# Performance work log

Hardware: AMD Instinct MI355X
Metric: run time of the kernel (lower is better)

## Reference

```python
import jax, jax.numpy as jnp
import numpy as np

DIM = 192
HEADS = 6
WH, WW = 7, 7
N = WH * WW            # 49 tokens per window
NW = 64                # windows per image
B = 64                 # images
B_ = NW * B            # 4096 window-batches
HEAD_DIM = DIM // HEADS
TABLE = (2 * WH - 1) * (2 * WW - 1)  # 169


def _relative_position_index():
    ch, cw = np.meshgrid(np.arange(WH), np.arange(WW), indexing='ij')
    coords = np.stack([ch, cw]).reshape(2, -1)          # (2, N)
    rel = coords[:, :, None] - coords[:, None, :]       # (2, N, N)
    rel = rel.transpose(1, 2, 0).astype(np.int32)
    rel[:, :, 0] += WH - 1
    rel[:, :, 1] += WW - 1
    rel[:, :, 0] *= 2 * WW - 1
    return jnp.asarray(rel.sum(-1))                     # (N, N) int32


def setup_inputs() -> dict:
    key = jax.random.key(0)
    ks = jax.random.split(key, 7)
    x = jax.random.normal(ks[0], (B_, N, DIM), dtype=jnp.float32)
    # 0 / -100 additive window mask (as produced by shifted-window masking)
    m = jax.random.uniform(ks[1], (NW, N, N))
    mask = jnp.where(m < 0.8, 0.0, -100.0).astype(jnp.float32)
    qkv_w = jax.random.normal(ks[2], (3 * DIM, DIM), dtype=jnp.float32) * 0.02
    qkv_b = jnp.zeros((3 * DIM,), dtype=jnp.float32)
    proj_w = jax.random.normal(ks[3], (DIM, DIM), dtype=jnp.float32) * 0.02
    proj_b = jnp.zeros((DIM,), dtype=jnp.float32)
    rpb_table = jax.random.normal(ks[4], (TABLE, HEADS), dtype=jnp.float32) * 0.02
    rel_idx = _relative_position_index()
    return {"x": x, "mask": mask, "qkv_w": qkv_w, "qkv_b": qkv_b,
            "proj_w": proj_w, "proj_b": proj_b, "rpb_table": rpb_table,
            "rel_idx": rel_idx}


def reference(x, mask, qkv_w, qkv_b, proj_w, proj_b, rpb_table, rel_idx):
    Bw, n, c = x.shape
    scale = HEAD_DIM ** -0.5
    qkv = x @ qkv_w.T + qkv_b                                  # (B_, N, 3C)
    qkv = qkv.reshape(Bw, n, 3, HEADS, HEAD_DIM).transpose(2, 0, 3, 1, 4)
    q, k, v = qkv[0], qkv[1], qkv[2]                           # (B_, H, N, hd)
    attn = jnp.einsum('bhid,bhjd->bhij', q * scale, k)          # (B_, H, N, N)
    bias = rpb_table[rel_idx.reshape(-1)].reshape(n, n, HEADS)  # gather
    attn = attn + bias.transpose(2, 0, 1)[None]                 # (1, H, N, N)
    nW = mask.shape[0]
    attn = attn.reshape(Bw // nW, nW, HEADS, n, n) + mask[None, :, None]
    attn = attn.reshape(Bw, HEADS, n, n)
    attn = jax.nn.softmax(attn, axis=-1).astype(v.dtype)
    out = jnp.einsum('bhij,bhjd->bhid', attn, v)                # (B_, H, N, hd)
    out = out.transpose(0, 2, 1, 3).reshape(Bw, n, c)
    return out @ proj_w.T + proj_b
```

## Files before the change

kernel.cpp:

```cpp
#include <hip/hip_runtime.h>

typedef unsigned short u16;
typedef unsigned int   u32;
typedef _Float16 f16x8 __attribute__((ext_vector_type(8)));
typedef __fp16   hf2   __attribute__((ext_vector_type(2)));
typedef float    f32x4 __attribute__((ext_vector_type(4)));

#define NTOK 49
#define CDIM 192
#define NH   6
#define HD   32
#define SC   0.17677669529663687f

#define QOFF   0
#define QSTR   200
#define KOFF   9800
#define VTOFF  19600
#define VTSTR  56
#define POFF   30352
#define PSTR   72
#define ARENA_U16 40152

#define WS_WQ 0
#define WS_WP 110592
#define WS_BM 147456

static __device__ __forceinline__ u16 f2h(float f){ union{ _Float16 h; u16 u;} v; v.h=(_Float16)f; return v.u; }
static __device__ __forceinline__ u32 pk2(float a, float b){
    hf2 h = __builtin_amdgcn_cvt_pkrtz(a, b);
    return __builtin_bit_cast(u32, h);
}

__global__ void prep_weights(const float* __restrict__ qkv_w,
                             const float* __restrict__ proj_w,
                             u16* __restrict__ ws)
{
    const int idx = blockIdx.x*256 + threadIdx.x;
    if (idx < 110592) {
        const int fid = idx >> 9, r = idx & 511;
        const int lane = r >> 3, e = r & 7;
        const int t = fid/6, k6 = fid - 6*t;
        const int col = t*16 + (lane & 15);
        const int kk  = k6*32 + (lane >> 4)*8 + e;
        float w = qkv_w[col*CDIM + kk];
        if (col < CDIM) w *= SC;
        ws[WS_WQ + idx] = f2h(w);
    } else if (idx < 147456) {
        const int j = idx - 110592;
        const int fid = j >> 9, r = j & 511;
        const int lane = r >> 3, e = r & 7;
        const int t = fid/6, k6 = fid - 6*t;
        const int col = t*16 + (lane & 15);
        const int kk  = k6*32 + (lane >> 4)*8 + e;
        ws[WS_WP + j] = f2h(proj_w[col*CDIM + kk]);
    }
}

__global__ void prep_bm(const float* __restrict__ mask,
                        const float* __restrict__ rpb,
                        const int*   __restrict__ rel,
                        u16* __restrict__ ws)
{
    const int idx = blockIdx.x*256 + threadIdx.x;
    if (idx >= 64*NH*256*16) return;
    const int r   = idx & 3;
    const int jt  = (idx >> 2) & 3;
    const int tid = (idx >> 4) & 255;
    const int rest = idx >> 12;
    const int h = rest % NH;
    const int w = rest / NH;
    const int i  = 16*(tid >> 6) + (tid & 15);
    const int lg = (tid >> 4) & 3;
    const int j  = jt*16 + 4*lg + r;
    float v;
    if (i >= NTOK)      v = 0.0f;
    else if (j >= NTOK) v = -1e30f;
    else v = rpb[rel[i*NTOK+j]*NH + h] + mask[((size_t)w*NTOK+i)*NTOK + j];
    ws[WS_BM + idx] = f2h(v);
}

#define LDFRAG(B, BASE, t) { const u16* _p = (BASE) + (size_t)(t)*3072 + lane*8;      \
    B[0]=*(const f16x8*)(_p);      B[1]=*(const f16x8*)(_p+512);                      \
    B[2]=*(const f16x8*)(_p+1024); B[3]=*(const f16x8*)(_p+1536);                     \
    B[4]=*(const f16x8*)(_p+2048); B[5]=*(const f16x8*)(_p+2560); }

#define QKV_STEP(s, CUR, NXT, PF) {                                                   \
    if (PF) LDFRAG(NXT, wq, t0+(s)+1);                                                \
    const int _t = t0+(s); const int _sec = _t/12; const int _cb = (_t - _sec*12)*16; \
    f32x4 _ac[2];                                                                     \
    if (_sec < 2) {       \
      float4 _b4 = *(const float4*)&qkv_b[_t*16 + 4*lg];                              \
      if (_sec == 0) { _b4.x*=SC; _b4.y*=SC; _b4.z*=SC; _b4.w*=SC; }                  \
      const f32x4 _ini = {_b4.x, _b4.y, _b4.z, _b4.w};                                \
      _ac[0]=_ini; _ac[1]=_ini;                                                       \
      _Pragma("unroll") for (int _k=0;_k<6;++_k)                                      \
        _Pragma("unroll") for (int _mi=0;_mi<2;++_mi)                                 \
          _ac[_mi] = __builtin_amdgcn_mfma_f32_16x16x32_f16(CUR[_k], A[_k][_mi], _ac[_mi],0,0,0); \
      u16* _dst = (_sec==0) ? (arena+QOFF) : (arena+KOFF);                            \
      _Pragma("unroll") for (int _mi=0;_mi<2;++_mi) {                                 \
        const int _tok = 32*mg + 16*_mi + l15;                                        \
        if (_tok < NTOK) {                                                            \
          uint2 _wd = make_uint2(pk2(_ac[_mi][0], _ac[_mi][1]),                       \
                                 pk2(_ac[_mi][2], _ac[_mi][3]));                      \
          *(uint2*)&_dst[_tok*QSTR + _cb + 4*lg] = _wd; } }                           \
    } else {                            \
      const float _b1 = qkv_b[384 + _cb + l15];                                       \
      const f32x4 _ini = {_b1, _b1, _b1, _b1};                                        \
      _ac[0]=_ini; _ac[1]=_ini;                                                       \
      _Pragma("unroll") for (int _k=0;_k<6;++_k)                                      \
        _Pragma("unroll") for (int _mi=0;_mi<2;++_mi)                                 \
          _ac[_mi] = __builtin_amdgcn_mfma_f32_16x16x32_f16(A[_k][_mi], CUR[_k], _ac[_mi],0,0,0); \
      _Pragma("unroll") for (int _mi=0;_mi<2;++_mi) {                                 \
        const int _tb = 32*mg + 16*_mi + 4*lg;                                        \
        if (_tb <= 48) {                                                              \
          uint2 _wd = make_uint2(pk2(_ac[_mi][0], _ac[_mi][1]),                       \
                                 pk2(_ac[_mi][2], _ac[_mi][3]));                      \
          *(uint2*)&arena[VTOFF + (_cb + l15)*VTSTR + _tb] = _wd; } } } }

#define PROJ_STEP(s, CUR, NXT, PF) {                                                  \
    if (PF) LDFRAG(NXT, wp, p0+(s)+1);                                                \
    const f32x4 _ini = {pb4[s].x, pb4[s].y, pb4[s].z, pb4[s].w};                      \
    f32x4 _ac[2]; _ac[0]=_ini; _ac[1]=_ini;                                           \
    _Pragma("unroll") for (int _k=0;_k<6;++_k)                                        \
      _Pragma("unroll") for (int _mi=0;_mi<2;++_mi)                                   \
        _ac[_mi] = __builtin_amdgcn_mfma_f32_16x16x32_f16(CUR[_k], PA[_k][_mi], _ac[_mi],0,0,0); \
    _Pragma("unroll") for (int _mi=0;_mi<2;++_mi) {                                   \
      const int _tok = 32*mg + 16*_mi + l15;                                          \
      if (_tok < NTOK) {                                                              \
        float4 _o = make_float4(_ac[_mi][0], _ac[_mi][1], _ac[_mi][2], _ac[_mi][3]);  \
        *(float4*)&og[(size_t)_tok*CDIM + (p0+(s))*16 + 4*lg] = _o; } } }

__global__ __launch_bounds__(512, 4)
void winattn_core(const float* __restrict__ x,
                  const float* __restrict__ qkv_b,
                  const float* __restrict__ proj_b,
                  const u16* __restrict__ ws,
                  float* __restrict__ out)
{
    __shared__ __align__(16) u16 arena[ARENA_U16];
    const int b    = blockIdx.x;
    const int tid  = threadIdx.x;
    const int lane = tid & 63;
    const int wv   = tid >> 6;
    const int rg   = wv & 3;
    const int mg   = wv >> 2;
    const int l15  = lane & 15;
    const int lg   = lane >> 4;
    const int win  = b & 63;

    {
        const float4* xg = (const float4*)(x + (size_t)b * (NTOK * CDIM));
        for (int i = tid; i < NTOK * CDIM / 4; i += 512) {
            const float4 v = xg[i];
            const int row = (i * 4) / CDIM, col = (i * 4) % CDIM;
            *(uint2*)&arena[POFF + row * QSTR + col] =
                make_uint2(pk2(v.x, v.y), pk2(v.z, v.w));
        }
        for (int i = tid; i < CDIM * 4; i += 512)
            arena[VTOFF + (i >> 2) * VTSTR + 52 + (i & 3)] = 0;
    }
    __syncthreads();

    const u16* wq = ws + WS_WQ;
    const int t0 = rg * 9;
    {
        f16x8 A[6][2];
        #pragma unroll
        for (int mi = 0; mi < 2; ++mi) {
            const int r = 32*mg + 16*mi + l15;
            const int ar = (r < NTOK ? r : NTOK-1) * QSTR;
            #pragma unroll
            for (int k6 = 0; k6 < 6; ++k6)
                A[k6][mi] = *(const f16x8*)&arena[POFF + ar + k6*32 + 8*lg];
        }
        f16x8 Ba[6], Bb[6];
        LDFRAG(Ba, wq, t0);
        QKV_STEP(0, Ba, Bb, 1)
        QKV_STEP(1, Bb, Ba, 1)
        QKV_STEP(2, Ba, Bb, 1)
        QKV_STEP(3, Bb, Ba, 1)
        QKV_STEP(4, Ba, Bb, 1)
        QKV_STEP(5, Bb, Ba, 1)
        QKV_STEP(6, Ba, Bb, 1)
        QKV_STEP(7, Bb, Ba, 1)
        QKV_STEP(8, Ba, Bb, 0)
    }

    f16x8 bmf[3][2];
    {
        const u16* bmb = ws + WS_BM + ((((size_t)win*NH + 3*mg)*256) + rg*64 + lane)*16;
        #pragma unroll
        for (int h3 = 0; h3 < 3; ++h3) {
            bmf[h3][0] = *(const f16x8*)(bmb + h3*4096);
            bmf[h3][1] = *(const f16x8*)(bmb + h3*4096 + 8);
        }
    }
    __syncthreads();

    const int i0 = 16 * rg;
    const bool myok = (i0 + l15 < NTOK);
    const int myrow = myok ? i0 + l15 : NTOK-1;
    int krow[4];
    #pragma unroll
    for (int jt = 0; jt < 4; ++jt)
        krow[jt] = (jt*16 + l15 < NTOK ? jt*16 + l15 : NTOK-1) * QSTR;

    f16x8 Qf[3];
    #pragma unroll
    for (int h3 = 0; h3 < 3; ++h3)
        Qf[h3] = *(const f16x8*)&arena[QOFF + myrow*QSTR + (3*mg+h3)*HD + 8*lg];

    u16* pp = arena + POFF + wv*1152;
    const int a1 = (32 + 8*lg <= 48) ? 32 + 8*lg : 48;

    #pragma unroll
    for (int h3 = 0; h3 < 3; ++h3) {
        const int h = 3*mg + h3;
        f32x4 pacc[4];
        #pragma unroll
        for (int jt = 0; jt < 4; ++jt) {
            const f16x8 Kf = *(const f16x8*)&arena[KOFF + krow[jt] + h*HD + 8*lg];
            f32x4 z = {};
            pacc[jt] = __builtin_amdgcn_mfma_f32_16x16x32_f16(Kf, Qf[h3], z, 0, 0, 0);
        }
        float val[4][4]; float mx = -3e38f;
        #pragma unroll
        for (int jt = 0; jt < 4; ++jt)
            #pragma unroll
            for (int r = 0; r < 4; ++r) {
                val[jt][r] = pacc[jt][r] + (float)bmf[h3][jt>>1][(jt&1)*4 + r];
                mx = fmaxf(mx, val[jt][r]);
            }
        mx = fmaxf(mx, __shfl_xor(mx, 16));
        mx = fmaxf(mx, __shfl_xor(mx, 32));
        float s = 0.f;
        #pragma unroll
        for (int jt = 0; jt < 4; ++jt)
            #pragma unroll
            for (int r = 0; r < 4; ++r) { const float e = __expf(val[jt][r]-mx); val[jt][r]=e; s+=e; }
        s += __shfl_xor(s, 16); s += __shfl_xor(s, 32);
        const float inv = 1.0f / s;
        #pragma unroll
        for (int jt = 0; jt < 4; ++jt)
            *(uint2*)&pp[l15*PSTR + jt*16 + 4*lg] =
                make_uint2(pk2(val[jt][0], val[jt][1]), pk2(val[jt][2], val[jt][3]));
        const f16x8 Pb0 = *(const f16x8*)&pp[l15*PSTR + 8*lg];
        const f16x8 Pb1 = *(const f16x8*)&pp[l15*PSTR + 32 + 8*lg];
        #pragma unroll
        for (int nt = 0; nt < 2; ++nt) {
            const int vr = (h*HD + nt*16 + l15) * VTSTR;
            const f16x8 Va0 = *(const f16x8*)&arena[VTOFF + vr + 8*lg];
            const f16x8 Va1 = *(const f16x8*)&arena[VTOFF + vr + a1];
            f32x4 o = {};
            o = __builtin_amdgcn_mfma_f32_16x16x32_f16(Va0, Pb0, o, 0, 0, 0);
            o = __builtin_amdgcn_mfma_f32_16x16x32_f16(Va1, Pb1, o, 0, 0, 0);
            if (myok) {
                *(uint2*)&arena[QOFF + (i0+l15)*QSTR + h*HD + nt*16 + 4*lg] =
                    make_uint2(pk2(o[0]*inv, o[1]*inv), pk2(o[2]*inv, o[3]*inv));
            }
        }
    }

    const u16* wp = ws + WS_WP;
    const int p0 = rg * 3;
    f16x8 Pa[6], Pb2[6];
    LDFRAG(Pa, wp, p0);
    float4 pb4[3];
    #pragma unroll
    for (int s = 0; s < 3; ++s)
        pb4[s] = *(const float4*)&proj_b[(p0+s)*16 + 4*lg];
    __syncthreads();
    {
        f16x8 PA[6][2];
        #pragma unroll
        for (int mi = 0; mi < 2; ++mi) {
            const int r = 32*mg + 16*mi + l15;
            const int ar = (r < NTOK ? r : NTOK-1) * QSTR;
            #pragma unroll
            for (int k6 = 0; k6 < 6; ++k6)
                PA[k6][mi] = *(const f16x8*)&arena[QOFF + ar + k6*32 + 8*lg];
        }
        float* og = out + (size_t)b * (NTOK * CDIM);
        PROJ_STEP(0, Pa, Pb2, 1)
        PROJ_STEP(1, Pb2, Pa, 1)
        PROJ_STEP(2, Pa, Pb2, 0)
    }
}

extern "C" void kernel_launch(void* const* d_in, const int* in_sizes, int n_in,
                              void* d_out, int out_size, void* d_ws, size_t ws_size,
                              hipStream_t stream) {
    const float* x      = (const float*)d_in[0];
    const float* mask   = (const float*)d_in[1];
    const float* qkv_w  = (const float*)d_in[2];
    const float* qkv_b  = (const float*)d_in[3];
    const float* proj_w = (const float*)d_in[4];
    const float* proj_b = (const float*)d_in[5];
    const float* rpb    = (const float*)d_in[6];
    const int*   rel    = (const int*)d_in[7];
    u16* ws = (u16*)d_ws;

    const int nwin = in_sizes[0] / (NTOK * CDIM);
    prep_weights<<<576, 256, 0, stream>>>(qkv_w, proj_w, ws);
    prep_bm<<<(64*NH*256*16 + 255)/256, 256, 0, stream>>>(mask, rpb, rel, ws);
    winattn_core<<<nwin, 512, 0, stream>>>(x, qkv_b, proj_b, ws, (float*)d_out);
}
```

Before: 185.1 us.

## Load x fragments directly from global, drop staging barrier, add MFMA priority hints

Input rows are now converted from global fp32 straight into MFMA A-fragments in registers. This removes the shared-memory staging of x and the __syncthreads that followed it, and it shrinks the LDS arena, which may allow higher occupancy. Bias is added after the MFMA chain instead of being used as the accumulator init, and sched_barrier plus s_setprio calls wrap the MFMA blocks so matrix work is prioritised over other waves. The trade-off is that each wave re-reads overlapping x rows from global memory, with less coalesced access and extra conversion work.

```diff
diff --git a/kernel.cpp b/kernel.cpp
--- a/kernel.cpp
+++ b/kernel.cpp
@@ -19,7 +19,7 @@
 #define VTSTR  56
 #define POFF   30352
 #define PSTR   72
-#define ARENA_U16 40152
+#define ARENA_U16 39568
 
 #define WS_WQ 0
 #define WS_WP 110592
@@ -85,45 +85,51 @@
     B[4]=*(const f16x8*)(_p+2048); B[5]=*(const f16x8*)(_p+2560); }
 
 #define QKV_STEP(s, CUR, NXT, PF) {                                                   \
-    if (PF) LDFRAG(NXT, wq, t0+(s)+1);                                                \
     const int _t = t0+(s); const int _sec = _t/12; const int _cb = (_t - _sec*12)*16; \
-    f32x4 _ac[2];                                                                     \
-    if (_sec < 2) {       \
-      float4 _b4 = *(const float4*)&qkv_b[_t*16 + 4*lg];                              \
-      if (_sec == 0) { _b4.x*=SC; _b4.y*=SC; _b4.z*=SC; _b4.w*=SC; }                  \
-      const f32x4 _ini = {_b4.x, _b4.y, _b4.z, _b4.w};                                \
-      _ac[0]=_ini; _ac[1]=_ini;                                                       \
+    if (PF) { LDFRAG(NXT, wq, t0+(s)+1); }                                            \
+    float4 _b4; float _b1;                                                            \
+    if (_sec < 2) { _b4 = *(const float4*)&qkv_b[_t*16 + 4*lg];                       \
+                    if (_sec == 0) { _b4.x*=SC; _b4.y*=SC; _b4.z*=SC; _b4.w*=SC; } }  \
+    else          { _b1 = qkv_b[384 + _cb + l15]; }                                   \
+    __builtin_amdgcn_sched_barrier(0);                                                \
+    f32x4 _ac[2] = {};                                                                \
+    __builtin_amdgcn_s_setprio(1);                                                    \
+    if (_sec < 2) {                         \
       _Pragma("unroll") for (int _k=0;_k<6;++_k)                                      \
         _Pragma("unroll") for (int _mi=0;_mi<2;++_mi)                                 \
           _ac[_mi] = __builtin_amdgcn_mfma_f32_16x16x32_f16(CUR[_k], A[_k][_mi], _ac[_mi],0,0,0); \
+    } else {                            \
+      _Pragma("unroll") for (int _k=0;_k<6;++_k)                                      \
+        _Pragma("unroll") for (int _mi=0;_mi<2;++_mi)                                 \
+          _ac[_mi] = __builtin_amdgcn_mfma_f32_16x16x32_f16(A[_k][_mi], CUR[_k], _ac[_mi],0,0,0); \
+    }                                                                                 \
+    __builtin_amdgcn_s_setprio(0);                                                    \
+    if (_sec < 2) {                                                                   \
       u16* _dst = (_sec==0) ? (arena+QOFF) : (arena+KOFF);                            \
       _Pragma("unroll") for (int _mi=0;_mi<2;++_mi) {                                 \
         const int _tok = 32*mg + 16*_mi + l15;                                        \
         if (_tok < NTOK) {                                                            \
-          uint2 _wd = make_uint2(pk2(_ac[_mi][0], _ac[_mi][1]),                       \
-                                 pk2(_ac[_mi][2], _ac[_mi][3]));                      \
+          uint2 _wd = make_uint2(pk2(_ac[_mi][0]+_b4.x, _ac[_mi][1]+_b4.y),           \
+                                 pk2(_ac[_mi][2]+_b4.z, _ac[_mi][3]+_b4.w));          \
           *(uint2*)&_dst[_tok*QSTR + _cb + 4*lg] = _wd; } }                           \
-    } else {                            \
-      const float _b1 = qkv_b[384 + _cb + l15];                                       \
-      const f32x4 _ini = {_b1, _b1, _b1, _b1};                                        \
-      _ac[0]=_ini; _ac[1]=_ini;                                                       \
-      _Pragma("unroll") for (int _k=0;_k<6;++_k)                                      \
-        _Pragma("unroll") for (int _mi=0;_mi<2;++_mi)                                 \
-          _ac[_mi] = __builtin_amdgcn_mfma_f32_16x16x32_f16(A[_k][_mi], CUR[_k], _ac[_mi],0,0,0); \
+    } else {                                                                          \
       _Pragma("unroll") for (int _mi=0;_mi<2;++_mi) {                                 \
         const int _tb = 32*mg + 16*_mi + 4*lg;                                        \
         if (_tb <= 48) {                                                              \
-          uint2 _wd = make_uint2(pk2(_ac[_mi][0], _ac[_mi][1]),                       \
-                                 pk2(_ac[_mi][2], _ac[_mi][3]));                      \
+          uint2 _wd = make_uint2(pk2(_ac[_mi][0]+_b1, _ac[_mi][1]+_b1),               \
+                                 pk2(_ac[_mi][2]+_b1, _ac[_mi][3]+_b1));              \
           *(uint2*)&arena[VTOFF + (_cb + l15)*VTSTR + _tb] = _wd; } } } }
 
 #define PROJ_STEP(s, CUR, NXT, PF) {                                                  \
-    if (PF) LDFRAG(NXT, wp, p0+(s)+1);                                                \
+    if (PF) { LDFRAG(NXT, wp, p0+(s)+1); }                                            \
+    __builtin_amdgcn_sched_barrier(0);                                                \
     const f32x4 _ini = {pb4[s].x, pb4[s].y, pb4[s].z, pb4[s].w};                      \
     f32x4 _ac[2]; _ac[0]=_ini; _ac[1]=_ini;                                           \
+    __builtin_amdgcn_s_setprio(1);                                                    \
     _Pragma("unroll") for (int _k=0;_k<6;++_k)                                        \
       _Pragma("unroll") for (int _mi=0;_mi<2;++_mi)                                   \
         _ac[_mi] = __builtin_amdgcn_mfma_f32_16x16x32_f16(CUR[_k], PA[_k][_mi], _ac[_mi],0,0,0); \
+    __builtin_amdgcn_s_setprio(0);                                                    \
     _Pragma("unroll") for (int _mi=0;_mi<2;++_mi) {                                   \
       const int _tok = 32*mg + 16*_mi + l15;                                          \
       if (_tok < NTOK) {                                                              \
@@ -148,33 +154,31 @@
     const int lg   = lane >> 4;
     const int win  = b & 63;
 
-    {
-        const float4* xg = (const float4*)(x + (size_t)b * (NTOK * CDIM));
-        for (int i = tid; i < NTOK * CDIM / 4; i += 512) {
-            const float4 v = xg[i];
-            const int row = (i * 4) / CDIM, col = (i * 4) % CDIM;
-            *(uint2*)&arena[POFF + row * QSTR + col] =
-                make_uint2(pk2(v.x, v.y), pk2(v.z, v.w));
-        }
-        for (int i = tid; i < CDIM * 4; i += 512)
-            arena[VTOFF + (i >> 2) * VTSTR + 52 + (i & 3)] = 0;
-    }
-    __syncthreads();
+    for (int i = tid; i < CDIM * 4; i += 512)
+        arena[VTOFF + (i >> 2) * VTSTR + 52 + (i & 3)] = 0;
 
     const u16* wq = ws + WS_WQ;
     const int t0 = rg * 9;
     {
-        f16x8 A[6][2];
-        #pragma unroll
-        for (int mi = 0; mi < 2; ++mi) {
-            const int r = 32*mg + 16*mi + l15;
-            const int ar = (r < NTOK ? r : NTOK-1) * QSTR;
-            #pragma unroll
-            for (int k6 = 0; k6 < 6; ++k6)
-                A[k6][mi] = *(const f16x8*)&arena[POFF + ar + k6*32 + 8*lg];
-        }
         f16x8 Ba[6], Bb[6];
         LDFRAG(Ba, wq, t0);
+        f16x8 A[6][2];
+        {
+            const float* xb = x + (size_t)b * (NTOK * CDIM);
+            #pragma unroll
+            for (int mi = 0; mi < 2; ++mi) {
+                const int r = 32*mg + 16*mi + l15;
+                const float* xr = xb + (size_t)(r < NTOK ? r : NTOK-1) * CDIM;
+                #pragma unroll
+                for (int k6 = 0; k6 < 6; ++k6) {
+                    const float4 f0 = *(const float4*)&xr[k6*32 + 8*lg];
+                    const float4 f1 = *(const float4*)&xr[k6*32 + 8*lg + 4];
+                    const uint4 u = make_uint4(pk2(f0.x,f0.y), pk2(f0.z,f0.w),
+                                               pk2(f1.x,f1.y), pk2(f1.z,f1.w));
+                    A[k6][mi] = __builtin_bit_cast(f16x8, u);
+                }
+            }
+        }
         QKV_STEP(0, Ba, Bb, 1)
         QKV_STEP(1, Bb, Ba, 1)
         QKV_STEP(2, Ba, Bb, 1)
@@ -246,17 +250,23 @@
                 make_uint2(pk2(val[jt][0], val[jt][1]), pk2(val[jt][2], val[jt][3]));
         const f16x8 Pb0 = *(const f16x8*)&pp[l15*PSTR + 8*lg];
         const f16x8 Pb1 = *(const f16x8*)&pp[l15*PSTR + 32 + 8*lg];
+        __builtin_amdgcn_s_setprio(1);
+        f32x4 o[2];
         #pragma unroll
         for (int nt = 0; nt < 2; ++nt) {
             const int vr = (h*HD + nt*16 + l15) * VTSTR;
             const f16x8 Va0 = *(const f16x8*)&arena[VTOFF + vr + 8*lg];
             const f16x8 Va1 = *(const f16x8*)&arena[VTOFF + vr + a1];
-            f32x4 o = {};
-            o = __builtin_amdgcn_mfma_f32_16x16x32_f16(Va0, Pb0, o, 0, 0, 0);
-            o = __builtin_amdgcn_mfma_f32_16x16x32_f16(Va1, Pb1, o, 0, 0, 0);
+            f32x4 z = {};
+            z = __builtin_amdgcn_mfma_f32_16x16x32_f16(Va0, Pb0, z, 0, 0, 0);
+            o[nt] = __builtin_amdgcn_mfma_f32_16x16x32_f16(Va1, Pb1, z, 0, 0, 0);
+        }
+        __builtin_amdgcn_s_setprio(0);
+        #pragma unroll
+        for (int nt = 0; nt < 2; ++nt) {
             if (myok) {
                 *(uint2*)&arena[QOFF + (i0+l15)*QSTR + h*HD + nt*16 + 4*lg] =
-                    make_uint2(pk2(o[0]*inv, o[1]*inv), pk2(o[2]*inv, o[3]*inv));
+                    make_uint2(pk2(o[nt][0]*inv, o[nt][1]*inv), pk2(o[nt][2]*inv, o[nt][3]*inv));
             }
         }
     }
@@ -269,17 +279,20 @@
     #pragma unroll
     for (int s = 0; s < 3; ++s)
         pb4[s] = *(const float4*)&proj_b[(p0+s)*16 + 4*lg];
+    int arow[2];
+    #pragma unroll
+    for (int mi = 0; mi < 2; ++mi) {
+        const int r = 32*mg + 16*mi + l15;
+        arow[mi] = (r < NTOK ? r : NTOK-1) * QSTR;
+    }
     __syncthreads();
     {
         f16x8 PA[6][2];
         #pragma unroll
-        for (int mi = 0; mi < 2; ++mi) {
-            const int r = 32*mg + 16*mi + l15;
-            const int ar = (r < NTOK ? r : NTOK-1) * QSTR;
+        for (int mi = 0; mi < 2; ++mi)
             #pragma unroll
             for (int k6 = 0; k6 < 6; ++k6)
-                PA[k6][mi] = *(const f16x8*)&arena[QOFF + ar + k6*32 + 8*lg];
-        }
+                PA[k6][mi] = *(const f16x8*)&arena[QOFF + arow[mi] + k6*32 + 8*lg];
         float* og = out + (size_t)b * (NTOK * CDIM);
         PROJ_STEP(0, Pa, Pb2, 1)
         PROJ_STEP(1, Pb2, Pa, 1)
```

After: 319.0 us. 72.3% more time.

## Halve block to 256 threads, deepen weight prefetch to three stages

Applied to the files above, without the earlier changes.

The fused window-attention kernel drops from 8 to 4 waves per block. Each wave now handles 18 QKV column tiles and 6 projection tiles, and in the attention phase it processes all 6 heads for one 16-row query tile. Weight fragments are prefetched three tiles ahead using four rotating register buffers instead of double buffering, so global-load latency is better hidden. The change also increases register pressure and lowers launch bounds to 256 threads with 2 blocks per SIMD, which cuts per-block parallelism and may reduce occupancy.

```diff
diff --git a/kernel.cpp b/kernel.cpp
--- a/kernel.cpp
+++ b/kernel.cpp
@@ -17,7 +17,7 @@
 #define KOFF   9800
 #define VTOFF  19600
 #define VTSTR  56
-#define POFF   30352
+#define XOFF   30352
 #define PSTR   72
 #define ARENA_U16 40152
 
@@ -85,7 +85,7 @@
     B[4]=*(const f16x8*)(_p+2048); B[5]=*(const f16x8*)(_p+2560); }
 
 #define QKV_STEP(s, CUR, NXT, PF) {                                                   \
-    if (PF) LDFRAG(NXT, wq, t0+(s)+1);                                                \
+    if (PF) { LDFRAG(NXT, wq, t0+(s)+3); }                                            \
     const int _t = t0+(s); const int _sec = _t/12; const int _cb = (_t - _sec*12)*16; \
     f32x4 _ac[2];                                                                     \
     if (_sec < 2) {       \
@@ -118,8 +118,9 @@
           *(uint2*)&arena[VTOFF + (_cb + l15)*VTSTR + _tb] = _wd; } } } }
 
 #define PROJ_STEP(s, CUR, NXT, PF) {                                                  \
-    if (PF) LDFRAG(NXT, wp, p0+(s)+1);                                                \
-    const f32x4 _ini = {pb4[s].x, pb4[s].y, pb4[s].z, pb4[s].w};                      \
+    if (PF) { LDFRAG(NXT, wp, p0+(s)+3); }                                            \
+    const float4 _pb = *(const float4*)&proj_b[(p0+(s))*16 + 4*lg];                   \
+    const f32x4 _ini = {_pb.x, _pb.y, _pb.z, _pb.w};                                  \
     f32x4 _ac[2]; _ac[0]=_ini; _ac[1]=_ini;                                           \
     _Pragma("unroll") for (int _k=0;_k<6;++_k)                                        \
       _Pragma("unroll") for (int _mi=0;_mi<2;++_mi)                                   \
@@ -130,7 +131,7 @@
         float4 _o = make_float4(_ac[_mi][0], _ac[_mi][1], _ac[_mi][2], _ac[_mi][3]);  \
         *(float4*)&og[(size_t)_tok*CDIM + (p0+(s))*16 + 4*lg] = _o; } } }
 
-__global__ __launch_bounds__(512, 4)
+__global__ __launch_bounds__(256, 2)
 void winattn_core(const float* __restrict__ x,
                   const float* __restrict__ qkv_b,
                   const float* __restrict__ proj_b,
@@ -142,27 +143,31 @@
     const int tid  = threadIdx.x;
     const int lane = tid & 63;
     const int wv   = tid >> 6;
-    const int rg   = wv & 3;
-    const int mg   = wv >> 2;
+    const int mg   = wv >> 1;
+    const int ng   = wv & 1;
     const int l15  = lane & 15;
     const int lg   = lane >> 4;
     const int win  = b & 63;
 
+    const u16* wq = ws + WS_WQ;
+    const int t0 = ng * 18;
+
+    f16x8 B0[6], B1[6], B2[6], B3[6];
+    LDFRAG(B0, wq, t0); LDFRAG(B1, wq, t0+1); LDFRAG(B2, wq, t0+2);
+
     {
         const float4* xg = (const float4*)(x + (size_t)b * (NTOK * CDIM));
-        for (int i = tid; i < NTOK * CDIM / 4; i += 512) {
+        for (int i = tid; i < NTOK * CDIM / 4; i += 256) {
             const float4 v = xg[i];
             const int row = (i * 4) / CDIM, col = (i * 4) % CDIM;
-            *(uint2*)&arena[POFF + row * QSTR + col] =
+            *(uint2*)&arena[XOFF + row * QSTR + col] =
                 make_uint2(pk2(v.x, v.y), pk2(v.z, v.w));
         }
-        for (int i = tid; i < CDIM * 4; i += 512)
-            arena[VTOFF + (i >> 2) * VTSTR + 52 + (i & 3)] = 0;
+        for (int i = tid; i < CDIM * 7; i += 256)
+            arena[VTOFF + (i / 7) * VTSTR + 49 + (i % 7)] = 0;
     }
     __syncthreads();
 
-    const u16* wq = ws + WS_WQ;
-    const int t0 = rg * 9;
     {
         f16x8 A[6][2];
         #pragma unroll
@@ -171,33 +176,40 @@
             const int ar = (r < NTOK ? r : NTOK-1) * QSTR;
             #pragma unroll
             for (int k6 = 0; k6 < 6; ++k6)
-                A[k6][mi] = *(const f16x8*)&arena[POFF + ar + k6*32 + 8*lg];
-        }
-        f16x8 Ba[6], Bb[6];
-        LDFRAG(Ba, wq, t0);
-        QKV_STEP(0, Ba, Bb, 1)
-        QKV_STEP(1, Bb, Ba, 1)
-        QKV_STEP(2, Ba, Bb, 1)
-        QKV_STEP(3, Bb, Ba, 1)
-        QKV_STEP(4, Ba, Bb, 1)
-        QKV_STEP(5, Bb, Ba, 1)
-        QKV_STEP(6, Ba, Bb, 1)
-        QKV_STEP(7, Bb, Ba, 1)
-        QKV_STEP(8, Ba, Bb, 0)
-    }
-
-    f16x8 bmf[3][2];
+                A[k6][mi] = *(const f16x8*)&arena[XOFF + ar + k6*32 + 8*lg];
+        }
+        QKV_STEP( 0, B0, B3, 1)
+        QKV_STEP( 1, B1, B0, 1)
+        QKV_STEP( 2, B2, B1, 1)
+        QKV_STEP( 3, B3, B2, 1)
+        QKV_STEP( 4, B0, B3, 1)
+        QKV_STEP( 5, B1, B0, 1)
+        QKV_STEP( 6, B2, B1, 1)
+        QKV_STEP( 7, B3, B2, 1)
+        QKV_STEP( 8, B0, B3, 1)
+        QKV_STEP( 9, B1, B0, 1)
+        QKV_STEP(10, B2, B1, 1)
+        QKV_STEP(11, B3, B2, 1)
+        QKV_STEP(12, B0, B3, 1)
+        QKV_STEP(13, B1, B0, 1)
+        QKV_STEP(14, B2, B1, 1)
+        QKV_STEP(15, B3, B2, 0)
+        QKV_STEP(16, B0, B3, 0)
+        QKV_STEP(17, B1, B0, 0)
+    }
+
+    f16x8 bmf[6][2];
     {
-        const u16* bmb = ws + WS_BM + ((((size_t)win*NH + 3*mg)*256) + rg*64 + lane)*16;
-        #pragma unroll
-        for (int h3 = 0; h3 < 3; ++h3) {
-            bmf[h3][0] = *(const f16x8*)(bmb + h3*4096);
-            bmf[h3][1] = *(const f16x8*)(bmb + h3*4096 + 8);
+        const u16* bmb = ws + WS_BM + (((size_t)win*NH)*256 + tid)*16;
+        #pragma unroll
+        for (int h = 0; h < NH; ++h) {
+            bmf[h][0] = *(const f16x8*)(bmb + h*4096);
+            bmf[h][1] = *(const f16x8*)(bmb + h*4096 + 8);
         }
     }
     __syncthreads();
 
-    const int i0 = 16 * rg;
+    const int i0 = 16 * wv;
     const bool myok = (i0 + l15 < NTOK);
     const int myrow = myok ? i0 + l15 : NTOK-1;
     int krow[4];
@@ -205,30 +217,28 @@
     for (int jt = 0; jt < 4; ++jt)
         krow[jt] = (jt*16 + l15 < NTOK ? jt*16 + l15 : NTOK-1) * QSTR;
 
-    f16x8 Qf[3];
+    f16x8 Qf[6];
     #pragma unroll
-    for (int h3 = 0; h3 < 3; ++h3)
-        Qf[h3] = *(const f16x8*)&arena[QOFF + myrow*QSTR + (3*mg+h3)*HD + 8*lg];
-
-    u16* pp = arena + POFF + wv*1152;
-    const int a1 = (32 + 8*lg <= 48) ? 32 + 8*lg : 48;
+    for (int h = 0; h < NH; ++h)
+        Qf[h] = *(const f16x8*)&arena[QOFF + myrow*QSTR + h*HD + 8*lg];
 
     #pragma unroll
-    for (int h3 = 0; h3 < 3; ++h3) {
-        const int h = 3*mg + h3;
+    for (int h = 0; h < NH; ++h) {
+        u16* pp = arena + XOFF + wv*2336 + (h & 1)*1168;
         f32x4 pacc[4];
         #pragma unroll
         for (int jt = 0; jt < 4; ++jt) {
             const f16x8 Kf = *(const f16x8*)&arena[KOFF + krow[jt] + h*HD + 8*lg];
             f32x4 z = {};
-            pacc[jt] = __builtin_amdgcn_mfma_f32_16x16x32_f16(Kf, Qf[h3], z, 0, 0, 0);
-        }
-        float val[4][4]; float mx = -3e38f;
+            pacc[jt] = __builtin_amdgcn_mfma_f32_16x16x32_f16(Kf, Qf[h], z, 0, 0, 0);
+        }
+        float val[4][4];
+        float mx = -3e38f;
         #pragma unroll
         for (int jt = 0; jt < 4; ++jt)
             #pragma unroll
             for (int r = 0; r < 4; ++r) {
-                val[jt][r] = pacc[jt][r] + (float)bmf[h3][jt>>1][(jt&1)*4 + r];
+                val[jt][r] = pacc[jt][r] + (float)bmf[h][jt>>1][(jt&1)*4 + r];
                 mx = fmaxf(mx, val[jt][r]);
             }
         mx = fmaxf(mx, __shfl_xor(mx, 16));
@@ -237,8 +247,12 @@
         #pragma unroll
         for (int jt = 0; jt < 4; ++jt)
             #pragma unroll
-            for (int r = 0; r < 4; ++r) { const float e = __expf(val[jt][r]-mx); val[jt][r]=e; s+=e; }
-        s += __shfl_xor(s, 16); s += __shfl_xor(s, 32);
+            for (int r = 0; r < 4; ++r) {
+                const float e = __expf(val[jt][r] - mx);
+                val[jt][r] = e; s += e;
+            }
+        s += __shfl_xor(s, 16);
+        s += __shfl_xor(s, 32);
         const float inv = 1.0f / s;
         #pragma unroll
         for (int jt = 0; jt < 4; ++jt)
@@ -246,6 +260,7 @@
                 make_uint2(pk2(val[jt][0], val[jt][1]), pk2(val[jt][2], val[jt][3]));
         const f16x8 Pb0 = *(const f16x8*)&pp[l15*PSTR + 8*lg];
         const f16x8 Pb1 = *(const f16x8*)&pp[l15*PSTR + 32 + 8*lg];
+        const int a1 = (32 + 8*lg <= 48) ? 32 + 8*lg : 48;
         #pragma unroll
         for (int nt = 0; nt < 2; ++nt) {
             const int vr = (h*HD + nt*16 + l15) * VTSTR;
@@ -262,28 +277,30 @@
     }
 
     const u16* wp = ws + WS_WP;
-    const int p0 = rg * 3;
-    f16x8 Pa[6], Pb2[6];
-    LDFRAG(Pa, wp, p0);
-    float4 pb4[3];
+    const int p0 = ng * 6;
+    f16x8 P0[6], P1[6], P2[6], P3[6];
+    LDFRAG(P0, wp, p0); LDFRAG(P1, wp, p0+1); LDFRAG(P2, wp, p0+2);
+    int arow[2];
     #pragma unroll
-    for (int s = 0; s < 3; ++s)
-        pb4[s] = *(const float4*)&proj_b[(p0+s)*16 + 4*lg];
+    for (int mi = 0; mi < 2; ++mi) {
+        const int r = 32*mg + 16*mi + l15;
+        arow[mi] = (r < NTOK ? r : NTOK-1) * QSTR;
+    }
     __syncthreads();
     {
         f16x8 PA[6][2];
         #pragma unroll
-        for (int mi = 0; mi < 2; ++mi) {
-            const int r = 32*mg + 16*mi + l15;
-            const int ar = (r < NTOK ? r : NTOK-1) * QSTR;
+        for (int mi = 0; mi < 2; ++mi)
             #pragma unroll
             for (int k6 = 0; k6 < 6; ++k6)
-                PA[k6][mi] = *(const f16x8*)&arena[QOFF + ar + k6*32 + 8*lg];
-        }
+                PA[k6][mi] = *(const f16x8*)&arena[QOFF + arow[mi] + k6*32 + 8*lg];
         float* og = out + (size_t)b * (NTOK * CDIM);
-        PROJ_STEP(0, Pa, Pb2, 1)
-        PROJ_STEP(1, Pb2, Pa, 1)
-        PROJ_STEP(2, Pa, Pb2, 0)
+        PROJ_STEP(0, P0, P3, 1)
+        PROJ_STEP(1, P1, P0, 1)
+        PROJ_STEP(2, P2, P1, 1)
+        PROJ_STEP(3, P3, P2, 0)
+        PROJ_STEP(4, P0, P3, 0)
+        PROJ_STEP(5, P1, P0, 0)
     }
 }
 
@@ -303,5 +320,5 @@
     const int nwin = in_sizes[0] / (NTOK * CDIM);
     prep_weights<<<576, 256, 0, stream>>>(qkv_w, proj_w, ws);
     prep_bm<<<(64*NH*256*16 + 255)/256, 256, 0, stream>>>(mask, rpb, rel, ws);
-    winattn_core<<<nwin, 512, 0, stream>>>(x, qkv_b, proj_b, ws, (float*)d_out);
-}
+    winattn_core<<<nwin, 256, 0, stream>>>(x, qkv_b, proj_b, ws, (float*)d_out);
+}
```

New measurement: 222.9 us. +20.4%, slower.
